# Kernel optimization log

Measured on AMD Instinct MI355X. Metric: run time of the kernel, lower is better.

## Reference

```python
import jax, jax.numpy as jnp
import numpy as np

BETA = 1.0
DIAG_REG = 1e-6
EPS = 1e-8
PSD_EPS = 1e-10  # torchaudio PSD mask-normalization eps

B, C, F, T = 4, 8, 512, 1000


def _trace(x):
    # trace over last two dims, shape (...,)
    return jnp.einsum('...ii->...', x)


def _psd(spec, mask):
    # spec: (B, C, F, T) complex; mask: (B, F, T) real
    # torchaudio PSD with normalize=True: time-normalized masked covariance
    m = mask / (jnp.sum(mask, axis=-1, keepdims=True) + PSD_EPS)
    m = m.astype(spec.dtype)
    # (B, F, C, C)
    return jnp.einsum('bcft,bft,beft->bfce', spec, m, jnp.conj(spec))


def setup_inputs() -> dict:
    key = jax.random.key(0)
    k1, k2, k3, k4 = jax.random.split(key, 4)
    return {
        'input_re': jax.random.normal(k1, (B, C, F, T), dtype=jnp.float32),
        'input_im': jax.random.normal(k2, (B, C, F, T), dtype=jnp.float32),
        'mask_s': jax.random.uniform(k3, (B, F, T), dtype=jnp.float32),
        'mask_n': jax.random.uniform(k4, (B, F, T), dtype=jnp.float32),
    }


def reference(input_re, input_im, mask_s, mask_n):
    x = (input_re + 1j * input_im).astype(jnp.complex64)  # (B, C, F, T)
    psd_s = _psd(x, mask_s)  # (B, F, C, C)
    psd_n = _psd(x, mask_n)  # (B, F, C, C)
    c = psd_n.shape[-1]
    # diagonal regularization: psd_n + (diag_reg * tr(psd_n).real + eps) * I
    d = DIAG_REG * _trace(psd_n).real + EPS  # (B, F)
    psd_n_reg = psd_n + d[..., None, None].astype(psd_n.dtype) * jnp.eye(c, dtype=psd_n.dtype)
    # rank-one parametric MWF, eq. (18) in Souden et al. 2010:
    # W = psd_n^{-1} psd_s / (beta + tr(psd_n^{-1} psd_s))
    num = jnp.linalg.solve(psd_n_reg, psd_s)  # (B, F, C, C)
    W = num / (BETA + _trace(num)[..., None, None])
    # MIMO filter output (ref_channel is None): (B, M=C, F, T)
    out = jnp.einsum('bfcm,bcft->bmft', jnp.conj(W), x)
    return out
```

## Files before the change

### kernel.cpp

```cpp
#include <hip/hip_runtime.h>


#define NB 4
#define NC 8
#define NF 512
#define NT 1000

__global__ __launch_bounds__(256, 2) void pmwf_kernel(
    const float* __restrict__ xre, const float* __restrict__ xim,
    const float* __restrict__ msk_s, const float* __restrict__ msk_n,
    float* __restrict__ out, int real_only)
{
    __shared__ float2 xs[NC * NT];
    __shared__ float2 M[8][16];
    __shared__ float2 invs;
    __shared__ float2 redscr[4];

    const int tid = threadIdx.x;
    const int bid = blockIdx.x;
    const int b = bid >> 9;
    const int f = bid & 511;

    const size_t mbase = ((size_t)b * NF + f) * NT;

    float2 psum = make_float2(0.f, 0.f);
    if (tid < 250) {
        const int t0 = tid * 4;
        float4 s4 = *(const float4*)(msk_s + mbase + t0);
        float4 n4 = *(const float4*)(msk_n + mbase + t0);
        psum.x = s4.x + s4.y + s4.z + s4.w;
        psum.y = n4.x + n4.y + n4.z + n4.w;
#pragma unroll
        for (int c = 0; c < NC; ++c) {
            const size_t xb = (((size_t)b * NC + c) * NF + f) * NT + t0;
            float4 r4 = *(const float4*)(xre + xb);
            float4 i4 = *(const float4*)(xim + xb);
            float2* xp = &xs[c * NT + t0];
            xp[0] = make_float2(r4.x, i4.x);
            xp[1] = make_float2(r4.y, i4.y);
            xp[2] = make_float2(r4.z, i4.z);
            xp[3] = make_float2(r4.w, i4.w);
        }
    }
#pragma unroll
    for (int d = 1; d < 64; d <<= 1) {
        psum.x += __shfl_xor(psum.x, d);
        psum.y += __shfl_xor(psum.y, d);
    }
    if ((tid & 63) == 0) redscr[tid >> 6] = psum;
    __syncthreads();
    if (tid == 0) {
        float ss = redscr[0].x + redscr[1].x + redscr[2].x + redscr[3].x;
        float sn = redscr[0].y + redscr[1].y + redscr[2].y + redscr[3].y;
        invs = make_float2(1.f / (ss + 1e-10f), 1.f / (sn + 1e-10f));
    }
    __syncthreads();

    {
        const int pair = tid >> 2;
        const int chunk = tid & 3;
        const int pc = pair >> 3, pe = pair & 7;
        const float2* xcp = &xs[pc * NT + chunk * 250];
        const float2* xep = &xs[pe * NT + chunk * 250];
        const float* msp = msk_s + mbase + chunk * 250;
        const float* mnp = msk_n + mbase + chunk * 250;
        float sre = 0.f, sim = 0.f, nre = 0.f, nim = 0.f;
#pragma unroll 5
        for (int i = 0; i < 250; ++i) {
            float2 a = xcp[i];
            float2 e = xep[i];
            float ms = msp[i];
            float mn = mnp[i];
            float pr = a.x * e.x + a.y * e.y;
            float pi = a.y * e.x - a.x * e.y;
            sre += ms * pr; sim += ms * pi;
            nre += mn * pr; nim += mn * pi;
        }
        sre += __shfl_xor(sre, 1); sre += __shfl_xor(sre, 2);
        sim += __shfl_xor(sim, 1); sim += __shfl_xor(sim, 2);
        nre += __shfl_xor(nre, 1); nre += __shfl_xor(nre, 2);
        nim += __shfl_xor(nim, 1); nim += __shfl_xor(nim, 2);
        if (chunk == 0) {
            float2 iv = invs;
            M[pc][pe]     = make_float2(nre * iv.y, nim * iv.y);
            M[pc][pe + 8] = make_float2(sre * iv.x, sim * iv.x);
        }
    }
    __syncthreads();

    float dreg;
    {
        float trn = 0.f;
#pragma unroll
        for (int k = 0; k < 8; ++k) trn += M[k][k].x;
        dreg = 1e-6f * trn + 1e-8f;
    }
    __syncthreads();
    if (tid < 8) M[tid][tid].x += dreg;
    __syncthreads();

    {
        const int r = tid >> 4, jc = tid & 15;
        const bool act = tid < 128;
#pragma unroll
        for (int k = 0; k < 8; ++k) {
            float2 newkj;
            if (act && r == k) {
                float2 p = M[k][k];
                float ip = 1.f / (p.x * p.x + p.y * p.y);
                float2 v = M[k][jc];
                newkj = make_float2((v.x * p.x + v.y * p.y) * ip,
                                    (v.y * p.x - v.x * p.y) * ip);
            }
            __syncthreads();
            if (act && r == k) M[k][jc] = newkj;
            __syncthreads();
            float2 fr, pv, cur;
            if (act) { fr = M[r][k]; pv = M[k][jc]; cur = M[r][jc]; }
            __syncthreads();
            if (act && r != k) {
                M[r][jc] = make_float2(cur.x - (fr.x * pv.x - fr.y * pv.y),
                                       cur.y - (fr.x * pv.y + fr.y * pv.x));
            }
            __syncthreads();
        }
    }

    {
        float2 tr = make_float2(1.f, 0.f);
#pragma unroll
        for (int k = 0; k < 8; ++k) { tr.x += M[k][k + 8].x; tr.y += M[k][k + 8].y; }
        float id = 1.f / (tr.x * tr.x + tr.y * tr.y);
        float2 invd = make_float2(tr.x * id, -tr.y * id);
        if (tid < 64) {
            int m = tid & 7, c = tid >> 3;
            float2 v = M[c][m + 8];
            M[m][c] = make_float2(v.x * invd.x - v.y * invd.y,
                                  -(v.x * invd.y + v.y * invd.x));
        }
    }
    __syncthreads();

    {
        const size_t obase = ((size_t)b * NC * NF + f) * NT;
        if (real_only) {
            for (int t = tid; t < NT; t += 256) {
                float2 xv[8];
#pragma unroll
                for (int c = 0; c < 8; ++c) xv[c] = xs[c * NT + t];
#pragma unroll
                for (int m = 0; m < 8; ++m) {
                    float ar = 0.f;
#pragma unroll
                    for (int c2 = 0; c2 < 8; ++c2) {
                        float2 g = M[m][c2];
                        float2 v = xv[c2];
                        ar += g.x * v.x - g.y * v.y;
                    }
                    out[obase + (size_t)m * NF * NT + t] = ar;
                }
            }
        } else {
            float2* outc = (float2*)out;
            for (int t = tid; t < NT; t += 256) {
                float2 xv[8];
#pragma unroll
                for (int c = 0; c < 8; ++c) xv[c] = xs[c * NT + t];
#pragma unroll
                for (int m = 0; m < 8; ++m) {
                    float ar = 0.f, ai = 0.f;
#pragma unroll
                    for (int c2 = 0; c2 < 8; ++c2) {
                        float2 g = M[m][c2];
                        float2 v = xv[c2];
                        ar += g.x * v.x - g.y * v.y;
                        ai += g.x * v.y + g.y * v.x;
                    }
                    outc[obase + (size_t)m * NF * NT + t] = make_float2(ar, ai);
                }
            }
        }
    }
}

extern "C" void kernel_launch(void* const* d_in, const int* in_sizes, int n_in,
                              void* d_out, int out_size, void* d_ws, size_t ws_size,
                              hipStream_t stream) {
    const float* xre = (const float*)d_in[0];
    const float* xim = (const float*)d_in[1];
    const float* ms  = (const float*)d_in[2];
    const float* mn  = (const float*)d_in[3];
    const int real_only = (out_size < 2 * NB * NC * NF * NT) ? 1 : 0;
    hipLaunchKernelGGL(pmwf_kernel, dim3(NB * NF), dim3(256), 0, stream,
                       xre, xim, ms, mn, (float*)d_out, real_only);
}
```

Baseline: 252.3 us.

## Stream x through shared memory in time passes with register-tiled covariance accumulation

Replaces the full 64KB shared buffer of the whole (C,T) slice with 256-sample passes, which cuts LDS use so four blocks can fit per CU instead of two. Each thread now accumulates a 2x2 channel-pair tile, reusing loaded x values across four outer products. Masks are cached in LDS as float2, and the partial sums are reduced across lanes and waves. The final filter application reads x again from global memory instead of LDS, which adds a second pass over the input in exchange for the higher occupancy.

```diff
diff --git a/kernel.cpp b/kernel.cpp
--- a/kernel.cpp
+++ b/kernel.cpp
@@ -5,23 +5,31 @@
 #define NC 8
 #define NF 512
 #define NT 1000
-
-__global__ __launch_bounds__(256, 2) void pmwf_kernel(
+#define CH ((size_t)(NF * NT))
+#define PASS_T 256
+#define XSTR 258
+
+__global__ __launch_bounds__(256, 4) void pmwf_kernel(
     const float* __restrict__ xre, const float* __restrict__ xim,
     const float* __restrict__ msk_s, const float* __restrict__ msk_n,
     float* __restrict__ out, int real_only)
 {
-    __shared__ float2 xs[NC * NT];
+    __shared__ float2 xs[NC * XSTR];
+    __shared__ float2 msn[NT];
     __shared__ float2 M[8][16];
+    __shared__ float  scr[4][16][16];
     __shared__ float2 invs;
     __shared__ float2 redscr[4];
 
-    const int tid = threadIdx.x;
-    const int bid = blockIdx.x;
+    const int tid  = threadIdx.x;
+    const int lane = tid & 63;
+    const int wave = tid >> 6;
+    const int bid  = blockIdx.x;
     const int b = bid >> 9;
     const int f = bid & 511;
 
     const size_t mbase = ((size_t)b * NF + f) * NT;
+    const size_t xbase = (size_t)b * NC * CH + (size_t)f * NT;
 
     float2 psum = make_float2(0.f, 0.f);
     if (tid < 250) {
@@ -30,61 +38,104 @@
         float4 n4 = *(const float4*)(msk_n + mbase + t0);
         psum.x = s4.x + s4.y + s4.z + s4.w;
         psum.y = n4.x + n4.y + n4.z + n4.w;
-#pragma unroll
-        for (int c = 0; c < NC; ++c) {
-            const size_t xb = (((size_t)b * NC + c) * NF + f) * NT + t0;
-            float4 r4 = *(const float4*)(xre + xb);
-            float4 i4 = *(const float4*)(xim + xb);
-            float2* xp = &xs[c * NT + t0];
-            xp[0] = make_float2(r4.x, i4.x);
-            xp[1] = make_float2(r4.y, i4.y);
-            xp[2] = make_float2(r4.z, i4.z);
-            xp[3] = make_float2(r4.w, i4.w);
-        }
+        msn[t0 + 0] = make_float2(s4.x, n4.x);
+        msn[t0 + 1] = make_float2(s4.y, n4.y);
+        msn[t0 + 2] = make_float2(s4.z, n4.z);
+        msn[t0 + 3] = make_float2(s4.w, n4.w);
     }
 #pragma unroll
     for (int d = 1; d < 64; d <<= 1) {
         psum.x += __shfl_xor(psum.x, d);
         psum.y += __shfl_xor(psum.y, d);
     }
-    if ((tid & 63) == 0) redscr[tid >> 6] = psum;
+    if (lane == 0) redscr[wave] = psum;
     __syncthreads();
     if (tid == 0) {
         float ss = redscr[0].x + redscr[1].x + redscr[2].x + redscr[3].x;
         float sn = redscr[0].y + redscr[1].y + redscr[2].y + redscr[3].y;
         invs = make_float2(1.f / (ss + 1e-10f), 1.f / (sn + 1e-10f));
     }
-    __syncthreads();
-
-    {
-        const int pair = tid >> 2;
-        const int chunk = tid & 3;
-        const int pc = pair >> 3, pe = pair & 7;
-        const float2* xcp = &xs[pc * NT + chunk * 250];
-        const float2* xep = &xs[pe * NT + chunk * 250];
-        const float* msp = msk_s + mbase + chunk * 250;
-        const float* mnp = msk_n + mbase + chunk * 250;
-        float sre = 0.f, sim = 0.f, nre = 0.f, nim = 0.f;
-#pragma unroll 5
-        for (int i = 0; i < 250; ++i) {
-            float2 a = xcp[i];
-            float2 e = xep[i];
-            float ms = msp[i];
-            float mn = mnp[i];
-            float pr = a.x * e.x + a.y * e.y;
-            float pi = a.y * e.x - a.x * e.y;
-            sre += ms * pr; sim += ms * pi;
-            nre += mn * pr; nim += mn * pi;
-        }
-        sre += __shfl_xor(sre, 1); sre += __shfl_xor(sre, 2);
-        sim += __shfl_xor(sim, 1); sim += __shfl_xor(sim, 2);
-        nre += __shfl_xor(nre, 1); nre += __shfl_xor(nre, 2);
-        nim += __shfl_xor(nim, 1); nim += __shfl_xor(nim, 2);
-        if (chunk == 0) {
-            float2 iv = invs;
-            M[pc][pe]     = make_float2(nre * iv.y, nim * iv.y);
-            M[pc][pe + 8] = make_float2(sre * iv.x, sim * iv.x);
-        }
+
+    const int tile  = tid & 15;
+    const int chunk = tid >> 4;
+    const int pcb = (tile >> 2) * 2;
+    const int peb = (tile & 3) * 2;
+
+    float aNr[4] = {0,0,0,0}, aNi[4] = {0,0,0,0};
+    float aSr[4] = {0,0,0,0}, aSi[4] = {0,0,0,0};
+
+    for (int p = 0; p < 4; ++p) {
+        const int tbeg  = p * PASS_T;
+        const int tpass = (p == 3) ? (NT - 3 * PASS_T) : PASS_T;
+        __syncthreads();
+#pragma unroll
+        for (int k = 0; k < 2; ++k) {
+            const int q = tid + (k << 8);
+            const int c = q >> 6;
+            const int tq = (q & 63) << 2;
+            if (tq < tpass) {
+                float4 r4 = *(const float4*)(xre + xbase + c * CH + tbeg + tq);
+                float4 i4 = *(const float4*)(xim + xbase + c * CH + tbeg + tq);
+                float2* xp = &xs[c * XSTR + tq];
+                xp[0] = make_float2(r4.x, i4.x);
+                xp[1] = make_float2(r4.y, i4.y);
+                xp[2] = make_float2(r4.z, i4.z);
+                xp[3] = make_float2(r4.w, i4.w);
+            }
+        }
+        __syncthreads();
+#pragma unroll
+        for (int i = 0; i < 16; ++i) {
+            const int tl = (i << 4) + chunk;
+            if (tl < tpass) {
+                float2 m2 = msn[tbeg + tl];
+                float2 a0 = xs[(pcb + 0) * XSTR + tl];
+                float2 a1 = xs[(pcb + 1) * XSTR + tl];
+                float2 e0 = xs[(peb + 0) * XSTR + tl];
+                float2 e1 = xs[(peb + 1) * XSTR + tl];
+                {   float pr = a0.x*e0.x + a0.y*e0.y, pi = a0.y*e0.x - a0.x*e0.y;
+                    aSr[0] += m2.x*pr; aSi[0] += m2.x*pi; aNr[0] += m2.y*pr; aNi[0] += m2.y*pi; }
+                {   float pr = a0.x*e1.x + a0.y*e1.y, pi = a0.y*e1.x - a0.x*e1.y;
+                    aSr[1] += m2.x*pr; aSi[1] += m2.x*pi; aNr[1] += m2.y*pr; aNi[1] += m2.y*pi; }
+                {   float pr = a1.x*e0.x + a1.y*e0.y, pi = a1.y*e0.x - a1.x*e0.y;
+                    aSr[2] += m2.x*pr; aSi[2] += m2.x*pi; aNr[2] += m2.y*pr; aNi[2] += m2.y*pi; }
+                {   float pr = a1.x*e1.x + a1.y*e1.y, pi = a1.y*e1.x - a1.x*e1.y;
+                    aSr[3] += m2.x*pr; aSi[3] += m2.x*pi; aNr[3] += m2.y*pr; aNi[3] += m2.y*pi; }
+            }
+        }
+    }
+
+#pragma unroll
+    for (int j = 0; j < 4; ++j) {
+        aNr[j] += __shfl_xor(aNr[j], 16); aNr[j] += __shfl_xor(aNr[j], 32);
+        aNi[j] += __shfl_xor(aNi[j], 16); aNi[j] += __shfl_xor(aNi[j], 32);
+        aSr[j] += __shfl_xor(aSr[j], 16); aSr[j] += __shfl_xor(aSr[j], 32);
+        aSi[j] += __shfl_xor(aSi[j], 16); aSi[j] += __shfl_xor(aSi[j], 32);
+    }
+    if (lane < 16) {
+#pragma unroll
+        for (int j = 0; j < 4; ++j) {
+            scr[wave][lane][j * 4 + 0] = aNr[j];
+            scr[wave][lane][j * 4 + 1] = aNi[j];
+            scr[wave][lane][j * 4 + 2] = aSr[j];
+            scr[wave][lane][j * 4 + 3] = aSi[j];
+        }
+    }
+    __syncthreads();
+    {
+        const int t2 = tid >> 4, slot = tid & 15;
+        float v = scr[0][t2][slot] + scr[1][t2][slot] + scr[2][t2][slot] + scr[3][t2][slot];
+        const int j = slot >> 2, kind = slot & 3;
+        const int pc = (t2 >> 2) * 2 + (j >> 1);
+        const int pe = (t2 & 3) * 2 + (j & 1);
+        float* Mf = (float*)M;
+        const float2 iv = invs;
+        const int baseN = (pc * 16 + pe) * 2;
+        const int baseS = (pc * 16 + pe + 8) * 2;
+        if      (kind == 0) Mf[baseN + 0] = v * iv.y;
+        else if (kind == 1) Mf[baseN + 1] = v * iv.y;
+        else if (kind == 2) Mf[baseS + 0] = v * iv.x;
+        else                Mf[baseS + 1] = v * iv.x;
     }
     __syncthreads();
 
@@ -130,8 +181,8 @@
         float2 tr = make_float2(1.f, 0.f);
 #pragma unroll
         for (int k = 0; k < 8; ++k) { tr.x += M[k][k + 8].x; tr.y += M[k][k + 8].y; }
-        float id = 1.f / (tr.x * tr.x + tr.y * tr.y);
-        float2 invd = make_float2(tr.x * id, -tr.y * id);
+        float idn = 1.f / (tr.x * tr.x + tr.y * tr.y);
+        float2 invd = make_float2(tr.x * idn, -tr.y * idn);
         if (tid < 64) {
             int m = tid & 7, c = tid >> 3;
             float2 v = M[c][m + 8];
@@ -142,41 +193,43 @@
     __syncthreads();
 
     {
-        const size_t obase = ((size_t)b * NC * NF + f) * NT;
+        const int m0 = wave * 2, m1 = m0 + 1;
+        float2 g0[8], g1[8];
+#pragma unroll
+        for (int c = 0; c < 8; ++c) { g0[c] = M[m0][c]; g1[c] = M[m1][c]; }
         if (real_only) {
-            for (int t = tid; t < NT; t += 256) {
-                float2 xv[8];
-#pragma unroll
-                for (int c = 0; c < 8; ++c) xv[c] = xs[c * NT + t];
-#pragma unroll
-                for (int m = 0; m < 8; ++m) {
-                    float ar = 0.f;
-#pragma unroll
-                    for (int c2 = 0; c2 < 8; ++c2) {
-                        float2 g = M[m][c2];
-                        float2 v = xv[c2];
-                        ar += g.x * v.x - g.y * v.y;
+            for (int it = 0; it < 16; ++it) {
+                const int t = (it << 6) + lane;
+                if (t < NT) {
+                    float r0 = 0.f, r1 = 0.f;
+#pragma unroll
+                    for (int c = 0; c < 8; ++c) {
+                        float vr = xre[xbase + c * CH + t];
+                        float vi = xim[xbase + c * CH + t];
+                        r0 += g0[c].x * vr - g0[c].y * vi;
+                        r1 += g1[c].x * vr - g1[c].y * vi;
                     }
-                    out[obase + (size_t)m * NF * NT + t] = ar;
+                    out[xbase + (size_t)m0 * CH + t] = r0;
+                    out[xbase + (size_t)m1 * CH + t] = r1;
                 }
             }
         } else {
             float2* outc = (float2*)out;
-            for (int t = tid; t < NT; t += 256) {
-                float2 xv[8];
-#pragma unroll
-                for (int c = 0; c < 8; ++c) xv[c] = xs[c * NT + t];
-#pragma unroll
-                for (int m = 0; m < 8; ++m) {
-                    float ar = 0.f, ai = 0.f;
-#pragma unroll
-                    for (int c2 = 0; c2 < 8; ++c2) {
-                        float2 g = M[m][c2];
-                        float2 v = xv[c2];
-                        ar += g.x * v.x - g.y * v.y;
-                        ai += g.x * v.y + g.y * v.x;
+            for (int it = 0; it < 16; ++it) {
+                const int t = (it << 6) + lane;
+                if (t < NT) {
+                    float r0 = 0.f, i0 = 0.f, r1 = 0.f, i1 = 0.f;
+#pragma unroll
+                    for (int c = 0; c < 8; ++c) {
+                        float vr = xre[xbase + c * CH + t];
+                        float vi = xim[xbase + c * CH + t];
+                        r0 += g0[c].x * vr - g0[c].y * vi;
+                        i0 += g0[c].x * vi + g0[c].y * vr;
+                        r1 += g1[c].x * vr - g1[c].y * vi;
+                        i1 += g1[c].x * vi + g1[c].y * vr;
                     }
-                    outc[obase + (size_t)m * NF * NT + t] = make_float2(ar, ai);
+                    outc[xbase + (size_t)m0 * CH + t] = make_float2(r0, i0);
+                    outc[xbase + (size_t)m1 * CH + t] = make_float2(r1, i1);
                 }
             }
         }
@@ -190,7 +243,7 @@
     const float* xim = (const float*)d_in[1];
     const float* ms  = (const float*)d_in[2];
     const float* mn  = (const float*)d_in[3];
-    const int real_only = (out_size < 2 * NB * NC * NF * NT) ? 1 : 0;
+    const int real_only = (out_size < (int)(2 * NB * NC * (size_t)NF * NT)) ? 1 : 0;
     hipLaunchKernelGGL(pmwf_kernel, dim3(NB * NF), dim3(256), 0, stream,
                        xre, xim, ms, mn, (float*)d_out, real_only);
 }
```

Measured after the change: 372.7 us. +47.7%, slower.
